# Performance work log

Measured on AMD Instinct MI355X. Metric: run time of the kernel, lower is better.

Reference implementation:

```python
import jax, jax.numpy as jnp
import numpy as np

D = 128        # hidden dim d
ED = 16        # edge_dim (Time2Vec width)
L = 2          # layers
N_BV, N_LT, N_CM, N_DN = 100000, 20000, 2000, 100000
E0, E1, E2, E3 = 600000, 200000, 500000, 200000
W_SCALE = 0.02


def setup_inputs() -> dict:
    key = jax.random.key(0)
    ks = jax.random.split(key, 24)
    rn = lambda i, s: jax.random.normal(ks[i], s, dtype=jnp.float32)
    ri = lambda i, e, hi: jax.random.randint(ks[i], (e,), 0, hi, dtype=jnp.int32)
    return {
        # node features per type
        "h_bv": rn(0, (N_BV, D)), "h_lt": rn(1, (N_LT, D)),
        "h_cm": rn(2, (N_CM, D)), "h_dn": rn(3, (N_DN, D)),
        # Time2Vec edge features per edge type
        "ft0": rn(4, (E0, ED)), "ft1": rn(5, (E1, ED)),
        "ft2": rn(6, (E2, ED)), "ft3": rn(7, (E3, ED)),
        # per-layer, per-edge-type conv Linear(2d, d)
        "conv_W": rn(8, (L, 4, 2 * D, D)) * W_SCALE,
        "conv_b": jnp.zeros((L, 4, D), jnp.float32),
        # per-edge-type edge MLP Linear(edge_dim, d)
        "emlp_W": rn(9, (4, ED, D)) * W_SCALE,
        "emlp_b": jnp.zeros((4, D), jnp.float32),
        # per-node-type LayerNorm params (order: bv, lt, cm, dn)
        "ln_g": jnp.ones((4, D), jnp.float32),
        "ln_b": jnp.zeros((4, D), jnp.float32),
        # edge indices (src -> dst): voted_on lt->bv, rev_read cm->bv,
        # donated_to dn->lt, read bv->cm
        "src0": ri(10, E0, N_LT), "dst0": ri(11, E0, N_BV),
        "src1": ri(12, E1, N_CM), "dst1": ri(13, E1, N_BV),
        "src2": ri(14, E2, N_DN), "dst2": ri(15, E2, N_LT),
        "src3": ri(16, E3, N_BV), "dst3": ri(17, E3, N_CM),
    }


def _seg_mean(x, idx, n):
    # scatter_mean: segment sum divided by counts (empty segments -> 0)
    s = jax.ops.segment_sum(x, idx, num_segments=n)
    c = jax.ops.segment_sum(jnp.ones((idx.shape[0],), x.dtype), idx, num_segments=n)
    return s / jnp.maximum(c, 1.0)[:, None]


def _layernorm(x, g, b, eps=1e-5):
    m = jnp.mean(x, -1, keepdims=True)
    v = jnp.var(x, -1, keepdims=True)
    return (x - m) * jax.lax.rsqrt(v + eps) * g + b


def reference(h_bv, h_lt, h_cm, h_dn, ft0, ft1, ft2, ft3,
              conv_W, conv_b, emlp_W, emlp_b, ln_g, ln_b,
              src0, dst0, src1, dst1, src2, dst2, src3, dst3):
    # node-type order: 0=bill_version, 1=legislator_term, 2=committee, 3=donor
    h = [h_bv, h_lt, h_cm, h_dn]
    # (et_idx, src_nt, dst_nt, src_idx, dst_idx, edge_time_feat)
    edges = [(0, 1, 0, src0, dst0, ft0),
             (1, 2, 0, src1, dst1, ft1),
             (2, 3, 1, src2, dst2, ft2),
             (3, 0, 2, src3, dst3, ft3)]
    n_layers = conv_W.shape[0]
    for l in range(n_layers):
        out = [jnp.zeros_like(x) for x in h]
        for (e, si, di, src, dst, ft) in edges:
            n_dst = h[di].shape[0]
            agg = _seg_mean(h[si][src], dst, n_dst)          # [N_dst, d]
            cat = jnp.concatenate([h[di], agg], axis=-1)     # [N_dst, 2d]
            y = cat @ conv_W[l, e] + conv_b[l, e]            # [N_dst, d]
            bias = ft @ emlp_W[e] + emlp_b[e]                # [E, d]
            y = y + _seg_mean(bias, dst, n_dst)
            out[di] = out[di] + y
        # drop=0.0 -> dropout is identity
        h = [_layernorm(out[i], ln_g[i], ln_b[i]) for i in range(4)]
    return tuple(h)
```

## Files before the change

### kernel.cpp

```cpp
#include <hip/hip_runtime.h>

typedef short v8s __attribute__((ext_vector_type(8)));
typedef float v4f __attribute__((ext_vector_type(4)));

#define S_I 100352

#define DEG_B   0ull
#define OFF_B   1605632ull
#define CUR_B   3211264ull
#define CSRS_B  4816896ull
#define FTS_B   16817152ull
#define BSUM_B  31025152ull
#define BPRE_B  31033344ull
#define WT_B    31041536ull
#define WEXT_B  31500288ull
#define VROW_B  31598592ull
#define AEXT_B  31599104ull
#define HA_B    47215104ull
#define ZA_B    104047104ull
#define HO_B    160879104ull
#define WS_NEEDED 192111104ull

__device__ __forceinline__ unsigned short f2bf(float f) {
    unsigned u = __float_as_uint(f);
    u += 0x7fffu + ((u >> 16) & 1u);
    return (unsigned short)(u >> 16);
}
__device__ __forceinline__ float bf2f(unsigned short h) {
    return __uint_as_float(((unsigned)h) << 16);
}

struct IPtr4 { const int* p[4]; };
struct IPtr8 { const int* s[4]; const int* d[4]; };
struct FPtr4 { const float* p[4]; };

__device__ __forceinline__ void edec(const IPtr8& sd, int i, int& li, int& eo,
                                     int& cb, int& d, int& s) {
    if (i < 600000)       { li = i;           eo = 0;       cb = 0;       d = sd.d[0][li]; s = sd.s[0][li]; }
    else if (i < 800000)  { li = i - 600000;  eo = 600000;  cb = S_I;     d = sd.d[1][li]; s = sd.s[1][li]; }
    else if (i < 1300000) { li = i - 800000;  eo = 800000;  cb = 2 * S_I; d = sd.d[2][li]; s = sd.s[2][li]; }
    else                  { li = i - 1300000; eo = 1300000; cb = 3 * S_I; d = sd.d[3][li]; s = sd.s[3][li]; }
}

__global__ void hist(IPtr4 dst, int* __restrict__ deg) {
    int base = blockIdx.x * 256 + threadIdx.x;
    if (base >= 375000) return;
    int d[4], cb[4];
#pragma unroll
    for (int k = 0; k < 4; k++) {
        int i = base + 375000 * k;
        if (i < 600000)       { cb[k] = 0;       d[k] = dst.p[0][i]; }
        else if (i < 800000)  { cb[k] = S_I;     d[k] = dst.p[1][i - 600000]; }
        else if (i < 1300000) { cb[k] = 2 * S_I; d[k] = dst.p[2][i - 800000]; }
        else                  { cb[k] = 3 * S_I; d[k] = dst.p[3][i - 1300000]; }
    }
#pragma unroll
    for (int k = 0; k < 4; k++) atomicAdd(&deg[cb[k] + d[k]], 1);
}

__device__ __forceinline__ void blk_decode(int b, int& e, int& lb, int& N) {
    if (b < 98)       { e = 0; lb = b;       N = 100000; }
    else if (b < 196) { e = 1; lb = b - 98;  N = 100000; }
    else if (b < 216) { e = 2; lb = b - 196; N = 20000;  }
    else              { e = 3; lb = b - 216; N = 2000;   }
}

__global__ void scan_p1(const int* __restrict__ deg, int* __restrict__ bsum) {
    int tid = threadIdx.x;
    int e, lb, N;
    blk_decode(blockIdx.x, e, lb, N);
    const int* dg = deg + e * S_I;
    int base = lb * 1024 + tid * 4;
    int s = 0;
#pragma unroll
    for (int j = 0; j < 4; j++) { int i = base + j; if (i < N) s += dg[i]; }
    for (int o = 32; o > 0; o >>= 1) s += __shfl_down(s, o);
    __shared__ int wsm[4];
    if ((tid & 63) == 0) wsm[tid >> 6] = s;
    __syncthreads();
    if (tid == 0) bsum[e * 512 + lb] = wsm[0] + wsm[1] + wsm[2] + wsm[3];
}

__global__ void scan_p2(const int* __restrict__ bsum, int* __restrict__ bpre, int* __restrict__ off) {
    __shared__ int sh[256];
    int tid = threadIdx.x;
    for (int e = 0; e < 4; e++) {
        int nb = (e < 2) ? 98 : (e == 2 ? 20 : 2);
        int N  = (e < 2) ? 100000 : (e == 2 ? 20000 : 2000);
        int v = (tid < nb) ? bsum[e * 512 + tid] : 0;
        sh[tid] = v;
        __syncthreads();
        for (int s = 1; s < 256; s <<= 1) {
            int t = (tid >= s) ? sh[tid - s] : 0;
            __syncthreads();
            sh[tid] += t;
            __syncthreads();
        }
        if (tid < nb) bpre[e * 512 + tid] = sh[tid] - v;
        if (tid == 0) off[e * S_I + N] = sh[255];
        __syncthreads();
    }
}

__global__ void scan_p3(const int* __restrict__ deg, const int* __restrict__ bpre,
                        int* __restrict__ off, int* __restrict__ cur) {
    int tid = threadIdx.x;
    int e, lb, N;
    blk_decode(blockIdx.x, e, lb, N);
    const int* dg = deg + e * S_I;
    int base = lb * 1024 + tid * 4;
    int v[4], s = 0;
#pragma unroll
    for (int j = 0; j < 4; j++) { int i = base + j; v[j] = (i < N) ? dg[i] : 0; s += v[j]; }
    int lane = tid & 63, w = tid >> 6;
    int sc = s;
    for (int d = 1; d < 64; d <<= 1) { int t = __shfl_up(sc, d); if (lane >= d) sc += t; }
    __shared__ int wsm[4];
    if (lane == 63) wsm[w] = sc;
    __syncthreads();
    int wpre = 0;
    for (int ww = 0; ww < 4; ww++) if (ww < w) wpre += wsm[ww];
    int run = bpre[e * 512 + lb] + wpre + (sc - s);
#pragma unroll
    for (int j = 0; j < 4; j++) {
        int i = base + j;
        if (i < N) { off[e * S_I + i] = run; cur[e * S_I + i] = run; }
        run += v[j];
    }
}

__global__ void fillcsr2(IPtr8 sd, int* __restrict__ cur, int2* __restrict__ csr2) {
    int base = blockIdx.x * 256 + threadIdx.x;
    if (base >= 375000) return;
    int li[4], eo[4], cb[4], d[4], s[4];
#pragma unroll
    for (int k = 0; k < 4; k++)
        edec(sd, base + 375000 * k, li[k], eo[k], cb[k], d[k], s[k]);
    int p[4];
#pragma unroll
    for (int k = 0; k < 4; k++)
        p[k] = atomicAdd(&cur[cb[k] + d[k]], 1);
#pragma unroll
    for (int k = 0; k < 4; k++)
        csr2[eo[k] + p[k]] = make_int2(s[k], li[k]);
}

__global__ __launch_bounds__(256) void ft_gather3(const int* __restrict__ off,
        const int2* __restrict__ csr2, FPtr4 ft, float* __restrict__ fts) {
    long long gid = (long long)blockIdx.x * 256 + threadIdx.x;
    int rid = (int)(gid >> 4), k = (int)(gid & 15);
    if (rid >= 222000) return;
    int e, n, eo;
    if (rid < 100000)      { e = 0; n = rid;          eo = 0; }
    else if (rid < 200000) { e = 1; n = rid - 100000; eo = 600000; }
    else if (rid < 220000) { e = 2; n = rid - 200000; eo = 800000; }
    else                   { e = 3; n = rid - 220000; eo = 1300000; }
    int s = off[e * S_I + n], en = off[e * S_I + n + 1];
    int dg = en - s;
    const int2* ep = csr2 + eo + s;
    const float* fp = ft.p[e];
    float a0 = 0.f, a1 = 0.f, a2 = 0.f, a3 = 0.f;
    int j = 0;
    for (; j + 4 <= dg; j += 4) {
        int e0 = ep[j].y, e1 = ep[j + 1].y, e2 = ep[j + 2].y, e3 = ep[j + 3].y;
        a0 += fp[(long long)e0 * 16 + k];
        a1 += fp[(long long)e1 * 16 + k];
        a2 += fp[(long long)e2 * 16 + k];
        a3 += fp[(long long)e3 * 16 + k];
    }
    if (j + 2 <= dg) {
        int e0 = ep[j].y, e1 = ep[j + 1].y;
        a0 += fp[(long long)e0 * 16 + k];
        a1 += fp[(long long)e1 * 16 + k];
        j += 2;
    }
    if (j < dg) a2 += fp[(long long)ep[j].y * 16 + k];
    fts[(long long)rid * 16 + k] = (a0 + a1) + (a2 + a3);
}

__global__ void const_build(const float* __restrict__ convW, const float* __restrict__ emlpW,
                            const float* __restrict__ emlpb, const float* __restrict__ convb,
                            const float* __restrict__ lnb, unsigned short* __restrict__ wt,
                            unsigned short* __restrict__ wext, float* __restrict__ vrow) {
    int gid = blockIdx.x * 256 + threadIdx.x;
    if (gid < 229376) {
        int i = gid;
        int l = i / 114688;
        int rem = i - l * 114688;
        int slot = rem >> 14;
        int idx = rem & 16383;
        int c = idx >> 7, k = idx & 127;
        float v;
        if (slot < 4)
            v = convW[((size_t)(l * 4 + slot) * 256 + 128 + k) * 128 + c];
        else if (slot == 4)
            v = convW[((size_t)(l * 4 + 0) * 256 + k) * 128 + c] +
                convW[((size_t)(l * 4 + 1) * 256 + k) * 128 + c];
        else
            v = convW[((size_t)(l * 4 + (slot - 3)) * 256 + k) * 128 + c];
        wt[i] = f2bf(v);
    } else if (gid < 229376 + 49152) {
        int g = gid - 229376;
        int slot = g >> 13;
        int rem = g & 8191;
        int c = rem >> 6, r = rem & 63;
        int l = slot / 3, t = slot - l * 3;
        int ef = (t == 0) ? 0 : (t == 1) ? 2 : 3;
        int rr = r & 31, half = r >> 5;
        int e = (t == 0) ? (half ? 1 : 0) : (half ? -1 : ef);
        float v = 0.f;
        if (e >= 0) {
            if (rr < 16)       v = emlpW[e * 2048 + rr * 128 + c];
            else if (rr == 16) v = emlpb[e * 128 + c];
        }
        if (r == 62) {
            v = convb[(l * 4 + ef) * 128 + c];
            if (t == 0) v += convb[(l * 4 + 1) * 128 + c];
        }
        wext[(long long)slot * 8192 + c * 64 + r] = f2bf(v);
    } else if (gid < 229376 + 49152 + 128) {
        int c = gid - 229376 - 49152;
        float s = 0.f;
        for (int k = 0; k < 128; k++)
            s += bf2f(f2bf(lnb[384 + k])) * bf2f(f2bf(convW[((size_t)(1 * 4 + 2) * 256 + 128 + k) * 128 + c]));
        vrow[c] = s;
    }
}

__global__ void aext_build(const int* __restrict__ off, const float* __restrict__ fts,
                           unsigned short* __restrict__ aext) {
    int gid = blockIdx.x * 256 + threadIdx.x;
    if (gid >= 7808000) return;
    int wid = gid >> 6, c = gid & 63;
    int t, n;
    if (wid < 100000)      { t = 0; n = wid; }
    else if (wid < 120000) { t = 1; n = wid - 100000; }
    else                   { t = 2; n = wid - 120000; }
    int cc = c & 31, half = c >> 5;
    int e = -1;
    if (t == 0) e = half ? 1 : 0;
    else if (half == 0) e = (t == 1) ? 2 : 3;
    float v = 0.f;
    if (e >= 0) {
        int s = off[e * S_I + n], en = off[e * S_I + n + 1];
        int dg = en - s;
        if (dg > 0) {
            int fb = (e == 0) ? 0 : (e == 1) ? 100000 : (e == 2) ? 200000 : 220000;
            if (cc < 16)       v = fts[(long long)(fb + n) * 16 + cc] / (float)dg;
            else if (cc == 16) v = 1.f;
        }
    }
    if (c == 62) v = 1.f;
    aext[(long long)wid * 64 + c] = f2bf(v);
}

__global__ void h0cvt(FPtr4 h, unsigned short* __restrict__ ha) {
    long long i4 = ((long long)blockIdx.x * 256 + threadIdx.x) * 4;
    if (i4 >= 28416000ll) return;
    long long r = i4 >> 7;
    int c = (int)(i4 & 127);
    int t; long long lr;
    if (r < 100000)      { t = 0; lr = r; }
    else if (r < 120000) { t = 1; lr = r - 100000; }
    else if (r < 122000) { t = 2; lr = r - 120000; }
    else                 { t = 3; lr = r - 122000; }
    const float4 v = *(const float4*)&h.p[t][lr * 128 + c];
    ushort4 o;
    o.x = f2bf(v.x); o.y = f2bf(v.y); o.z = f2bf(v.z); o.w = f2bf(v.w);
    *(ushort4*)&ha[i4] = o;
}

__device__ __forceinline__ void acc8(float* t, uint4 v) {
    t[0] += __uint_as_float(v.x << 16);
    t[1] += __uint_as_float(v.x & 0xffff0000u);
    t[2] += __uint_as_float(v.y << 16);
    t[3] += __uint_as_float(v.y & 0xffff0000u);
    t[4] += __uint_as_float(v.z << 16);
    t[5] += __uint_as_float(v.z & 0xffff0000u);
    t[6] += __uint_as_float(v.w << 16);
    t[7] += __uint_as_float(v.w & 0xffff0000u);
}

__global__ __launch_bounds__(256) void pull_all(int l, const int* __restrict__ off,
        const int2* __restrict__ csr2, const unsigned short* __restrict__ za,
        const float* __restrict__ vrow, unsigned short* __restrict__ hout) {
    long long gid = (long long)blockIdx.x * 256 + threadIdx.x;
    int wid = (int)(gid >> 6), lane = (int)(gid & 63);
    if (wid >= 122000) return;
    int t, n;
    if (wid < 100000)      { t = 0; n = wid; }
    else if (wid < 120000) { t = 1; n = wid - 100000; }
    else                   { t = 2; n = wid - 120000; }
    int sub = lane >> 4, k8 = (lane & 15) * 8;
    float a[8];
#pragma unroll
    for (int i = 0; i < 8; i++) a[i] = 0.f;
    int ef = (t == 0) ? 0 : (t == 1) ? 2 : 3;
    int ne = (t == 0) ? 2 : 1;
    for (int ii = 0; ii < ne; ii++) {
        int e = ef + ii;
        int s = off[e * S_I + n], en = off[e * S_I + n + 1];
        int cnt = en - s;
        if (cnt <= 0) continue;
        if (e == 2 && l == 1) {
            if (sub == 0) {
                float4 v0 = *(const float4*)&vrow[k8];
                float4 v1 = *(const float4*)&vrow[k8 + 4];
                a[0] += v0.x; a[1] += v0.y; a[2] += v0.z; a[3] += v0.w;
                a[4] += v1.x; a[5] += v1.y; a[6] += v1.z; a[7] += v1.w;
            }
            continue;
        }
        int eo   = (e == 0) ? 0 : (e == 1) ? 600000 : (e == 2) ? 800000 : 1300000;
        long long zo = (e == 0) ? 0 : (e == 1) ? 20000 : (e == 2) ? 22000 : 122000;
        const int2* cs = csr2 + eo + s;
        const unsigned short* zb = za + zo * 128;
        float t0[8], t1[8];
#pragma unroll
        for (int i = 0; i < 8; i++) { t0[i] = 0.f; t1[i] = 0.f; }
        int j = sub;
        for (; j + 4 < cnt; j += 8) {
            int i0 = cs[j].x, i1 = cs[j + 4].x;
            uint4 v0 = *(const uint4*)&zb[(long long)i0 * 128 + k8];
            uint4 v1 = *(const uint4*)&zb[(long long)i1 * 128 + k8];
            acc8(t0, v0);
            acc8(t1, v1);
        }
        if (j < cnt) {
            int i0 = cs[j].x;
            uint4 v0 = *(const uint4*)&zb[(long long)i0 * 128 + k8];
            acc8(t0, v0);
        }
        float inv = 1.f / (float)cnt;
#pragma unroll
        for (int i = 0; i < 8; i++) a[i] += (t0[i] + t1[i]) * inv;
    }
#pragma unroll
    for (int i = 0; i < 8; i++) {
        a[i] += __shfl_xor(a[i], 16);
        a[i] += __shfl_xor(a[i], 32);
    }
    if (sub == 0) {
        uint4 p;
        p.x = (unsigned)f2bf(a[0]) | ((unsigned)f2bf(a[1]) << 16);
        p.y = (unsigned)f2bf(a[2]) | ((unsigned)f2bf(a[3]) << 16);
        p.z = (unsigned)f2bf(a[4]) | ((unsigned)f2bf(a[5]) << 16);
        p.w = (unsigned)f2bf(a[6]) | ((unsigned)f2bf(a[7]) << 16);
        *(uint4*)&hout[(long long)wid * 128 + k8] = p;
    }
}

__global__ __launch_bounds__(256, 2) void zgemm(int l, const unsigned short* __restrict__ ha,
        const unsigned short* __restrict__ wt, unsigned short* __restrict__ za) {
    __shared__ unsigned short As[16384];
    __shared__ unsigned short Bs[16384];
    int b = blockIdx.x;
    int e, lb, M; long long aoff, zoff;
    if (l == 0) {
        if (b < 157)      { e = 0; lb = b;       M = 20000;  aoff = 100000; zoff = 0; }
        else if (b < 173) { e = 1; lb = b - 157; M = 2000;   aoff = 120000; zoff = 20000; }
        else if (b < 955) { e = 2; lb = b - 173; M = 100000; aoff = 122000; zoff = 22000; }
        else              { e = 3; lb = b - 955; M = 100000; aoff = 0;      zoff = 122000; }
    } else {
        if (b < 157)      { e = 0; lb = b;       M = 20000;  aoff = 100000; zoff = 0; }
        else if (b < 173) { e = 1; lb = b - 157; M = 2000;   aoff = 120000; zoff = 20000; }
        else              { e = 3; lb = b - 173; M = 100000; aoff = 0;      zoff = 122000; }
    }
    const unsigned short* A  = ha + aoff * 128;
    const unsigned short* Wt = wt + (size_t)(l * 7 + e) * 16384;
    unsigned short* outb = za + zoff * 128;
    int tid = threadIdx.x;
    long long row0 = (long long)lb * 128;
#pragma unroll
    for (int i = 0; i < 8; i++) {
        int idx = tid + i * 256;
        int m = idx >> 4, c = idx & 15;
        int sw = c ^ (m & 15);
        uint4 va = make_uint4(0u, 0u, 0u, 0u);
        long long gr = row0 + m;
        if (gr < M) va = *(const uint4*)&A[gr * 128 + c * 8];
        *(uint4*)&As[m * 128 + sw * 8] = va;
        uint4 wv = *(const uint4*)&Wt[m * 128 + c * 8];
        *(uint4*)&Bs[m * 128 + sw * 8] = wv;
    }
    __syncthreads();
    int lane = tid & 63, w = tid >> 6;
    int q = lane >> 4, ml = lane & 15;
    v4f acc[2][8];
#pragma unroll
    for (int i = 0; i < 2; i++)
#pragma unroll
        for (int j = 0; j < 8; j++) acc[i][j] = (v4f){0.f, 0.f, 0.f, 0.f};
#pragma unroll
    for (int kc = 0; kc < 4; kc++) {
        int ch = (4 * kc + q) ^ ml;
        v8s af[2], bf[8];
#pragma unroll
        for (int i = 0; i < 2; i++) af[i] = *(const v8s*)&As[(32 * w + 16 * i + ml) * 128 + ch * 8];
#pragma unroll
        for (int j = 0; j < 8; j++) bf[j] = *(const v8s*)&Bs[(16 * j + ml) * 128 + ch * 8];
#pragma unroll
        for (int i = 0; i < 2; i++)
#pragma unroll
            for (int j = 0; j < 8; j++)
                acc[i][j] = __builtin_amdgcn_mfma_f32_16x16x32_bf16(af[i], bf[j], acc[i][j], 0, 0, 0);
    }
#pragma unroll
    for (int i = 0; i < 2; i++)
#pragma unroll
        for (int r = 0; r < 4; r++) {
            long long row = row0 + 32 * w + 16 * i + q * 4 + r;
            if (row < M) {
#pragma unroll
                for (int j = 0; j < 8; j++)
                    outb[row * 128 + 16 * j + ml] = f2bf(acc[i][j][r]);
            }
        }
}

__global__ __launch_bounds__(256, 2) void selfgemm(int l, unsigned short* __restrict__ ha,
        const unsigned short* __restrict__ wt, const unsigned short* __restrict__ wext,
        const unsigned short* __restrict__ aext, const unsigned short* __restrict__ ho,
        float* __restrict__ outf, const float* __restrict__ lng, const float* __restrict__ lnb) {
    __shared__ unsigned short As[16384];
    __shared__ unsigned short Bs[16384];
    int b = blockIdx.x;
    int t, lb, M; long long hoff;
    if (b < 782)      { t = 0; lb = b;       M = 100000; hoff = 0; }
    else if (b < 939) { t = 1; lb = b - 782; M = 20000;  hoff = 100000; }
    else              { t = 2; lb = b - 939; M = 2000;   hoff = 120000; }
    const unsigned short* A    = ha + hoff * 128;
    const unsigned short* Ax   = aext + hoff * 64;
    const unsigned short* Wt_  = wt + (size_t)(l * 7 + 4 + t) * 16384;
    const unsigned short* Wx   = wext + (size_t)(l * 3 + t) * 8192;
    const unsigned short* Cadd = ho + hoff * 128;
    const float* g  = lng + t * 128;
    const float* bb = lnb + t * 128;
    int tid = threadIdx.x;
    long long row0 = (long long)lb * 128;
#pragma unroll
    for (int i = 0; i < 8; i++) {
        int idx = tid + i * 256;
        int m = idx >> 4, c = idx & 15;
        int sw = c ^ (m & 15);
        uint4 va = make_uint4(0u, 0u, 0u, 0u);
        long long gr = row0 + m;
        if (gr < M) va = *(const uint4*)&A[gr * 128 + c * 8];
        *(uint4*)&As[m * 128 + sw * 8] = va;
        uint4 wv = *(const uint4*)&Wt_[m * 128 + c * 8];
        *(uint4*)&Bs[m * 128 + sw * 8] = wv;
    }
    __syncthreads();
    int lane = tid & 63, w = tid >> 6;
    int q = lane >> 4, ml = lane & 15;
    v4f acc[2][8];
#pragma unroll
    for (int i = 0; i < 2; i++)
#pragma unroll
        for (int j = 0; j < 8; j++) acc[i][j] = (v4f){0.f, 0.f, 0.f, 0.f};
#pragma unroll
    for (int kc = 0; kc < 4; kc++) {
        int ch = (4 * kc + q) ^ ml;
        v8s af[2], bf[8];
#pragma unroll
        for (int i = 0; i < 2; i++) af[i] = *(const v8s*)&As[(32 * w + 16 * i + ml) * 128 + ch * 8];
#pragma unroll
        for (int j = 0; j < 8; j++) bf[j] = *(const v8s*)&Bs[(16 * j + ml) * 128 + ch * 8];
#pragma unroll
        for (int i = 0; i < 2; i++)
#pragma unroll
            for (int j = 0; j < 8; j++)
                acc[i][j] = __builtin_amdgcn_mfma_f32_16x16x32_bf16(af[i], bf[j], acc[i][j], 0, 0, 0);
    }
    __syncthreads();
#pragma unroll
    for (int i = 0; i < 4; i++) {
        int idx = tid + i * 256;
        int m = idx >> 3, c = idx & 7;
        int sw = c ^ (m & 7);
        uint4 va = make_uint4(0u, 0u, 0u, 0u);
        long long gr = row0 + m;
        if (gr < M) va = *(const uint4*)&Ax[gr * 64 + c * 8];
        *(uint4*)&As[m * 64 + sw * 8] = va;
        uint4 wv = *(const uint4*)&Wx[m * 64 + c * 8];
        *(uint4*)&Bs[m * 64 + sw * 8] = wv;
    }
    __syncthreads();
#pragma unroll
    for (int kc = 0; kc < 2; kc++) {
        int ch = (4 * kc + q) ^ (ml & 7);
        v8s af[2], bf[8];
#pragma unroll
        for (int i = 0; i < 2; i++) af[i] = *(const v8s*)&As[(32 * w + 16 * i + ml) * 64 + ch * 8];
#pragma unroll
        for (int j = 0; j < 8; j++) bf[j] = *(const v8s*)&Bs[(16 * j + ml) * 64 + ch * 8];
#pragma unroll
        for (int i = 0; i < 2; i++)
#pragma unroll
            for (int j = 0; j < 8; j++)
                acc[i][j] = __builtin_amdgcn_mfma_f32_16x16x32_bf16(af[i], bf[j], acc[i][j], 0, 0, 0);
    }
    float gv[8], bv[8];
#pragma unroll
    for (int j = 0; j < 8; j++) { gv[j] = g[16 * j + ml]; bv[j] = bb[16 * j + ml]; }
    unsigned short* outb = ha + hoff * 128;
    float* outF = outf + hoff * 128;
#pragma unroll
    for (int i = 0; i < 2; i++) {
#pragma unroll
        for (int r = 0; r < 4; r++) {
            long long row = row0 + 32 * w + 16 * i + q * 4 + r;
            bool valid = row < M;
            float s = 0.f, s2 = 0.f;
#pragma unroll
            for (int j = 0; j < 8; j++) {
                float v = acc[i][j][r];
                if (valid) v += bf2f(Cadd[row * 128 + 16 * j + ml]);
                acc[i][j][r] = v;
                s += v; s2 += v * v;
            }
#pragma unroll
            for (int msk = 1; msk < 16; msk <<= 1) {
                s  += __shfl_xor(s,  msk);
                s2 += __shfl_xor(s2, msk);
            }
            float mean = s * 0.0078125f;
            float var  = s2 * 0.0078125f - mean * mean;
            float rs = rsqrtf(var + 1e-5f);
            if (valid) {
#pragma unroll
                for (int j = 0; j < 8; j++) {
                    float v = (acc[i][j][r] - mean) * rs * gv[j] + bv[j];
                    if (l == 0) outb[row * 128 + 16 * j + ml] = f2bf(v);
                    else        outF[row * 128 + 16 * j + ml] = v;
                }
            }
        }
    }
}

__global__ void fill_dn(float* __restrict__ of, const float* __restrict__ lnb3) {
    long long i4 = ((long long)blockIdx.x * 256 + threadIdx.x) * 4;
    if (i4 >= 12800000ll) return;
    int c = (int)(i4 & 127);
    *(float4*)&of[i4] = make_float4(lnb3[c], lnb3[c + 1], lnb3[c + 2], lnb3[c + 3]);
}

extern "C" void kernel_launch(void* const* d_in, const int* in_sizes, int n_in,
                              void* d_out, int out_size, void* d_ws, size_t ws_size,
                              hipStream_t stream) {
    if (ws_size < WS_NEEDED) return;

    const float* h0[4] = {(const float*)d_in[0], (const float*)d_in[1],
                          (const float*)d_in[2], (const float*)d_in[3]};
    const float* ftp[4] = {(const float*)d_in[4], (const float*)d_in[5],
                           (const float*)d_in[6], (const float*)d_in[7]};
    const float* convW = (const float*)d_in[8];
    const float* convb = (const float*)d_in[9];
    const float* emlpW = (const float*)d_in[10];
    const float* emlpb = (const float*)d_in[11];
    const float* lng   = (const float*)d_in[12];
    const float* lnb   = (const float*)d_in[13];
    const int* srcp[4] = {(const int*)d_in[14], (const int*)d_in[16],
                          (const int*)d_in[18], (const int*)d_in[20]};
    const int* dstp[4] = {(const int*)d_in[15], (const int*)d_in[17],
                          (const int*)d_in[19], (const int*)d_in[21]};
    char* ws = (char*)d_ws;
    float* out = (float*)d_out;

    int* deg = (int*)(ws + DEG_B);
    int* off = (int*)(ws + OFF_B);
    int* cur = (int*)(ws + CUR_B);
    int2* csr2 = (int2*)(ws + CSRS_B);
    float* fts = (float*)(ws + FTS_B);
    int* bsum = (int*)(ws + BSUM_B);
    int* bpre = (int*)(ws + BPRE_B);
    unsigned short* wt   = (unsigned short*)(ws + WT_B);
    unsigned short* wext = (unsigned short*)(ws + WEXT_B);
    float* vrow = (float*)(ws + VROW_B);
    unsigned short* aext = (unsigned short*)(ws + AEXT_B);
    unsigned short* ha = (unsigned short*)(ws + HA_B);
    unsigned short* za = (unsigned short*)(ws + ZA_B);
    unsigned short* ho = (unsigned short*)(ws + HO_B);

    hipMemsetAsync(deg, 0, 4 * S_I * sizeof(int), stream);

    IPtr4 dsts; for (int e = 0; e < 4; e++) dsts.p[e] = dstp[e];
    hist<<<1465, 256, 0, stream>>>(dsts, deg);

    scan_p1<<<218, 256, 0, stream>>>(deg, bsum);
    scan_p2<<<1, 256, 0, stream>>>(bsum, bpre, off);
    scan_p3<<<218, 256, 0, stream>>>(deg, bpre, off, cur);
    IPtr8 sd;
    for (int e = 0; e < 4; e++) { sd.s[e] = srcp[e]; sd.d[e] = dstp[e]; }
    fillcsr2<<<1465, 256, 0, stream>>>(sd, cur, csr2);

    FPtr4 ftq;  for (int e = 0; e < 4; e++) ftq.p[e] = ftp[e];
    ft_gather3<<<13875, 256, 0, stream>>>(off, csr2, ftq, fts);

    const_build<<<1089, 256, 0, stream>>>(convW, emlpW, emlpb, convb, lnb, wt, wext, vrow);
    FPtr4 hq; for (int t = 0; t < 4; t++) hq.p[t] = h0[t];
    h0cvt<<<27750, 256, 0, stream>>>(hq, ha);
    aext_build<<<30500, 256, 0, stream>>>(off, fts, aext);

    for (int l = 0; l < 2; l++) {
        zgemm<<<(l == 0) ? 1737 : 955, 256, 0, stream>>>(l, ha, wt, za);
        pull_all<<<30500, 256, 0, stream>>>(l, off, csr2, za, vrow, ho);
        selfgemm<<<955, 256, 0, stream>>>(l, ha, wt, wext, aext, ho, out, lng, lnb);
    }
    fill_dn<<<12500, 256, 0, stream>>>(out + 122000ll * 128, lnb + 384);
}
```

Baseline: 887.2 us.

## Merge independent stages into combined kernels to cut launches and overlap work

```diff
diff --git a/kernel.cpp b/kernel.cpp
--- a/kernel.cpp
+++ b/kernel.cpp
@@ -34,14 +34,6 @@
 struct IPtr8 { const int* s[4]; const int* d[4]; };
 struct FPtr4 { const float* p[4]; };
 
-__device__ __forceinline__ void edec(const IPtr8& sd, int i, int& li, int& eo,
-                                     int& cb, int& d, int& s) {
-    if (i < 600000)       { li = i;           eo = 0;       cb = 0;       d = sd.d[0][li]; s = sd.s[0][li]; }
-    else if (i < 800000)  { li = i - 600000;  eo = 600000;  cb = S_I;     d = sd.d[1][li]; s = sd.s[1][li]; }
-    else if (i < 1300000) { li = i - 800000;  eo = 800000;  cb = 2 * S_I; d = sd.d[2][li]; s = sd.s[2][li]; }
-    else                  { li = i - 1300000; eo = 1300000; cb = 3 * S_I; d = sd.d[3][li]; s = sd.s[3][li]; }
-}
-
 __global__ void hist(IPtr4 dst, int* __restrict__ deg) {
     int base = blockIdx.x * 256 + threadIdx.x;
     if (base >= 375000) return;
@@ -129,107 +121,280 @@
     }
 }
 
-__global__ void fillcsr2(IPtr8 sd, int* __restrict__ cur, int2* __restrict__ csr2) {
-    int base = blockIdx.x * 256 + threadIdx.x;
-    if (base >= 375000) return;
-    int li[4], eo[4], cb[4], d[4], s[4];
-#pragma unroll
-    for (int k = 0; k < 4; k++)
-        edec(sd, base + 375000 * k, li[k], eo[k], cb[k], d[k], s[k]);
-    int p[4];
-#pragma unroll
-    for (int k = 0; k < 4; k++)
-        p[k] = atomicAdd(&cur[cb[k] + d[k]], 1);
-#pragma unroll
-    for (int k = 0; k < 4; k++)
-        csr2[eo[k] + p[k]] = make_int2(s[k], li[k]);
-}
-
-__global__ __launch_bounds__(256) void ft_gather3(const int* __restrict__ off,
-        const int2* __restrict__ csr2, FPtr4 ft, float* __restrict__ fts) {
-    long long gid = (long long)blockIdx.x * 256 + threadIdx.x;
-    int rid = (int)(gid >> 4), k = (int)(gid & 15);
-    if (rid >= 222000) return;
-    int e, n, eo;
-    if (rid < 100000)      { e = 0; n = rid;          eo = 0; }
-    else if (rid < 200000) { e = 1; n = rid - 100000; eo = 600000; }
-    else if (rid < 220000) { e = 2; n = rid - 200000; eo = 800000; }
-    else                   { e = 3; n = rid - 220000; eo = 1300000; }
-    int s = off[e * S_I + n], en = off[e * S_I + n + 1];
-    int dg = en - s;
-    const int2* ep = csr2 + eo + s;
-    const float* fp = ft.p[e];
-    float a0 = 0.f, a1 = 0.f, a2 = 0.f, a3 = 0.f;
-    int j = 0;
-    for (; j + 4 <= dg; j += 4) {
-        int e0 = ep[j].y, e1 = ep[j + 1].y, e2 = ep[j + 2].y, e3 = ep[j + 3].y;
-        a0 += fp[(long long)e0 * 16 + k];
-        a1 += fp[(long long)e1 * 16 + k];
-        a2 += fp[(long long)e2 * 16 + k];
-        a3 += fp[(long long)e3 * 16 + k];
-    }
-    if (j + 2 <= dg) {
-        int e0 = ep[j].y, e1 = ep[j + 1].y;
-        a0 += fp[(long long)e0 * 16 + k];
-        a1 += fp[(long long)e1 * 16 + k];
-        j += 2;
-    }
-    if (j < dg) a2 += fp[(long long)ep[j].y * 16 + k];
-    fts[(long long)rid * 16 + k] = (a0 + a1) + (a2 + a3);
-}
-
-__global__ void const_build(const float* __restrict__ convW, const float* __restrict__ emlpW,
-                            const float* __restrict__ emlpb, const float* __restrict__ convb,
-                            const float* __restrict__ lnb, unsigned short* __restrict__ wt,
-                            unsigned short* __restrict__ wext, float* __restrict__ vrow) {
-    int gid = blockIdx.x * 256 + threadIdx.x;
-    if (gid < 229376) {
-        int i = gid;
-        int l = i / 114688;
-        int rem = i - l * 114688;
-        int slot = rem >> 14;
-        int idx = rem & 16383;
-        int c = idx >> 7, k = idx & 127;
-        float v;
-        if (slot < 4)
-            v = convW[((size_t)(l * 4 + slot) * 256 + 128 + k) * 128 + c];
-        else if (slot == 4)
-            v = convW[((size_t)(l * 4 + 0) * 256 + k) * 128 + c] +
-                convW[((size_t)(l * 4 + 1) * 256 + k) * 128 + c];
-        else
-            v = convW[((size_t)(l * 4 + (slot - 3)) * 256 + k) * 128 + c];
-        wt[i] = f2bf(v);
-    } else if (gid < 229376 + 49152) {
-        int g = gid - 229376;
-        int slot = g >> 13;
-        int rem = g & 8191;
-        int c = rem >> 6, r = rem & 63;
-        int l = slot / 3, t = slot - l * 3;
-        int ef = (t == 0) ? 0 : (t == 1) ? 2 : 3;
-        int rr = r & 31, half = r >> 5;
-        int e = (t == 0) ? (half ? 1 : 0) : (half ? -1 : ef);
-        float v = 0.f;
-        if (e >= 0) {
-            if (rr < 16)       v = emlpW[e * 2048 + rr * 128 + c];
-            else if (rr == 16) v = emlpb[e * 128 + c];
-        }
-        if (r == 62) {
-            v = convb[(l * 4 + ef) * 128 + c];
-            if (t == 0) v += convb[(l * 4 + 1) * 128 + c];
-        }
-        wext[(long long)slot * 8192 + c * 64 + r] = f2bf(v);
-    } else if (gid < 229376 + 49152 + 128) {
-        int c = gid - 229376 - 49152;
-        float s = 0.f;
-        for (int k = 0; k < 128; k++)
-            s += bf2f(f2bf(lnb[384 + k])) * bf2f(f2bf(convW[((size_t)(1 * 4 + 2) * 256 + 128 + k) * 128 + c]));
-        vrow[c] = s;
-    }
-}
-
-__global__ void aext_build(const int* __restrict__ off, const float* __restrict__ fts,
-                           unsigned short* __restrict__ aext) {
-    int gid = blockIdx.x * 256 + threadIdx.x;
+__global__ void mega1(IPtr8 sd, int* __restrict__ cur, int2* __restrict__ csr2,
+                      FPtr4 h, unsigned short* __restrict__ ha,
+                      const float* __restrict__ convW, const float* __restrict__ emlpW,
+                      const float* __restrict__ emlpb, const float* __restrict__ convb,
+                      const float* __restrict__ lnb, unsigned short* __restrict__ wt,
+                      unsigned short* __restrict__ wext, float* __restrict__ vrow) {
+    int b = blockIdx.x;
+    int tid = threadIdx.x;
+    if (b < 1465) {
+        int base = b * 256 + tid;
+        if (base >= 375000) return;
+        int li[4], eo[4], cb[4], d[4], s[4];
+#pragma unroll
+        for (int k = 0; k < 4; k++) {
+            int i = base + 375000 * k;
+            if (i < 600000)       { li[k] = i;           eo[k] = 0;       cb[k] = 0;       d[k] = sd.d[0][li[k]]; s[k] = sd.s[0][li[k]]; }
+            else if (i < 800000)  { li[k] = i - 600000;  eo[k] = 600000;  cb[k] = S_I;     d[k] = sd.d[1][li[k]]; s[k] = sd.s[1][li[k]]; }
+            else if (i < 1300000) { li[k] = i - 800000;  eo[k] = 800000;  cb[k] = 2 * S_I; d[k] = sd.d[2][li[k]]; s[k] = sd.s[2][li[k]]; }
+            else                  { li[k] = i - 1300000; eo[k] = 1300000; cb[k] = 3 * S_I; d[k] = sd.d[3][li[k]]; s[k] = sd.s[3][li[k]]; }
+        }
+        int p[4];
+#pragma unroll
+        for (int k = 0; k < 4; k++)
+            p[k] = atomicAdd(&cur[cb[k] + d[k]], 1);
+#pragma unroll
+        for (int k = 0; k < 4; k++)
+            csr2[eo[k] + p[k]] = make_int2(s[k], li[k]);
+    } else if (b < 29215) {
+        long long i4 = ((long long)(b - 1465) * 256 + tid) * 4;
+        if (i4 >= 28416000ll) return;
+        long long r = i4 >> 7;
+        int c = (int)(i4 & 127);
+        int t; long long lr;
+        if (r < 100000)      { t = 0; lr = r; }
+        else if (r < 120000) { t = 1; lr = r - 100000; }
+        else if (r < 122000) { t = 2; lr = r - 120000; }
+        else                 { t = 3; lr = r - 122000; }
+        const float4 v = *(const float4*)&h.p[t][lr * 128 + c];
+        ushort4 o;
+        o.x = f2bf(v.x); o.y = f2bf(v.y); o.z = f2bf(v.z); o.w = f2bf(v.w);
+        *(ushort4*)&ha[i4] = o;
+    } else {
+        int gid = (b - 29215) * 256 + tid;
+        if (gid < 229376) {
+            int i = gid;
+            int l = i / 114688;
+            int rem = i - l * 114688;
+            int slot = rem >> 14;
+            int idx = rem & 16383;
+            int c = idx >> 7, k = idx & 127;
+            float v;
+            if (slot < 4)
+                v = convW[((size_t)(l * 4 + slot) * 256 + 128 + k) * 128 + c];
+            else if (slot == 4)
+                v = convW[((size_t)(l * 4 + 0) * 256 + k) * 128 + c] +
+                    convW[((size_t)(l * 4 + 1) * 256 + k) * 128 + c];
+            else
+                v = convW[((size_t)(l * 4 + (slot - 3)) * 256 + k) * 128 + c];
+            wt[i] = f2bf(v);
+        } else if (gid < 229376 + 49152) {
+            int g = gid - 229376;
+            int slot = g >> 13;
+            int rem = g & 8191;
+            int c = rem >> 6, r = rem & 63;
+            int l = slot / 3, t = slot - l * 3;
+            int ef = (t == 0) ? 0 : (t == 1) ? 2 : 3;
+            int rr = r & 31, half = r >> 5;
+            int e = (t == 0) ? (half ? 1 : 0) : (half ? -1 : ef);
+            float v = 0.f;
+            if (e >= 0) {
+                if (rr < 16)       v = emlpW[e * 2048 + rr * 128 + c];
+                else if (rr == 16) v = emlpb[e * 128 + c];
+            }
+            if (r == 62) {
+                v = convb[(l * 4 + ef) * 128 + c];
+                if (t == 0) v += convb[(l * 4 + 1) * 128 + c];
+            }
+            wext[(long long)slot * 8192 + c * 64 + r] = f2bf(v);
+        } else if (gid < 229376 + 49152 + 128) {
+            int c = gid - 229376 - 49152;
+            float s = 0.f;
+            for (int k = 0; k < 128; k++)
+                s += bf2f(f2bf(lnb[384 + k])) * bf2f(f2bf(convW[((size_t)(1 * 4 + 2) * 256 + 128 + k) * 128 + c]));
+            vrow[c] = s;
+        }
+    }
+}
+
+__global__ __launch_bounds__(256, 2) void mega2(const unsigned short* __restrict__ ha,
+        const unsigned short* __restrict__ wt, unsigned short* __restrict__ za,
+        const int* __restrict__ off, const int2* __restrict__ csr2,
+        FPtr4 ft, float* __restrict__ fts) {
+    __shared__ unsigned short As[16384];
+    __shared__ unsigned short Bs[16384];
+    int tid = threadIdx.x;
+    if (blockIdx.x >= 1737) {
+        long long gid = (long long)(blockIdx.x - 1737) * 256 + tid;
+        int rid = (int)(gid >> 4), k = (int)(gid & 15);
+        if (rid >= 222000) return;
+        int e, n, eo;
+        if (rid < 100000)      { e = 0; n = rid;          eo = 0; }
+        else if (rid < 200000) { e = 1; n = rid - 100000; eo = 600000; }
+        else if (rid < 220000) { e = 2; n = rid - 200000; eo = 800000; }
+        else                   { e = 3; n = rid - 220000; eo = 1300000; }
+        int s = off[e * S_I + n], en = off[e * S_I + n + 1];
+        int dg = en - s;
+        const int2* ep = csr2 + eo + s;
+        const float* fp = ft.p[e];
+        float a0 = 0.f, a1 = 0.f, a2 = 0.f, a3 = 0.f;
+        int j = 0;
+        for (; j + 4 <= dg; j += 4) {
+            int e0 = ep[j].y, e1 = ep[j + 1].y, e2 = ep[j + 2].y, e3 = ep[j + 3].y;
+            a0 += fp[(long long)e0 * 16 + k];
+            a1 += fp[(long long)e1 * 16 + k];
+            a2 += fp[(long long)e2 * 16 + k];
+            a3 += fp[(long long)e3 * 16 + k];
+        }
+        if (j + 2 <= dg) {
+            int e0 = ep[j].y, e1 = ep[j + 1].y;
+            a0 += fp[(long long)e0 * 16 + k];
+            a1 += fp[(long long)e1 * 16 + k];
+            j += 2;
+        }
+        if (j < dg) a2 += fp[(long long)ep[j].y * 16 + k];
+        fts[(long long)rid * 16 + k] = (a0 + a1) + (a2 + a3);
+        return;
+    }
+    int b = blockIdx.x;
+    int e, lb, M; long long aoff, zoff;
+    if (b < 157)      { e = 0; lb = b;       M = 20000;  aoff = 100000; zoff = 0; }
+    else if (b < 173) { e = 1; lb = b - 157; M = 2000;   aoff = 120000; zoff = 20000; }
+    else if (b < 955) { e = 2; lb = b - 173; M = 100000; aoff = 122000; zoff = 22000; }
+    else              { e = 3; lb = b - 955; M = 100000; aoff = 0;      zoff = 122000; }
+    const unsigned short* A  = ha + aoff * 128;
+    const unsigned short* Wt = wt + (size_t)e * 16384;
+    unsigned short* outb = za + zoff * 128;
+    long long row0 = (long long)lb * 128;
+#pragma unroll
+    for (int i = 0; i < 8; i++) {
+        int idx = tid + i * 256;
+        int m = idx >> 4, c = idx & 15;
+        int sw = c ^ (m & 15);
+        uint4 va = make_uint4(0u, 0u, 0u, 0u);
+        long long gr = row0 + m;
+        if (gr < M) va = *(const uint4*)&A[gr * 128 + c * 8];
+        *(uint4*)&As[m * 128 + sw * 8] = va;
+        uint4 wv = *(const uint4*)&Wt[m * 128 + c * 8];
+        *(uint4*)&Bs[m * 128 + sw * 8] = wv;
+    }
+    __syncthreads();
+    int lane = tid & 63, w = tid >> 6;
+    int q = lane >> 4, ml = lane & 15;
+    v4f acc[2][8];
+#pragma unroll
+    for (int i = 0; i < 2; i++)
+#pragma unroll
+        for (int j = 0; j < 8; j++) acc[i][j] = (v4f){0.f, 0.f, 0.f, 0.f};
+#pragma unroll
+    for (int kc = 0; kc < 4; kc++) {
+        int ch = (4 * kc + q) ^ ml;
+        v8s af[2], bf[8];
+#pragma unroll
+        for (int i = 0; i < 2; i++) af[i] = *(const v8s*)&As[(32 * w + 16 * i + ml) * 128 + ch * 8];
+#pragma unroll
+        for (int j = 0; j < 8; j++) bf[j] = *(const v8s*)&Bs[(16 * j + ml) * 128 + ch * 8];
+#pragma unroll
+        for (int i = 0; i < 2; i++)
+#pragma unroll
+            for (int j = 0; j < 8; j++)
+                acc[i][j] = __builtin_amdgcn_mfma_f32_16x16x32_bf16(af[i], bf[j], acc[i][j], 0, 0, 0);
+    }
+#pragma unroll
+    for (int i = 0; i < 2; i++)
+#pragma unroll
+        for (int r = 0; r < 4; r++) {
+            long long row = row0 + 32 * w + 16 * i + q * 4 + r;
+            if (row < M) {
+#pragma unroll
+                for (int j = 0; j < 8; j++)
+                    outb[row * 128 + 16 * j + ml] = f2bf(acc[i][j][r]);
+            }
+        }
+}
+
+__device__ __forceinline__ void acc8(float* t, uint4 v) {
+    t[0] += __uint_as_float(v.x << 16);
+    t[1] += __uint_as_float(v.x & 0xffff0000u);
+    t[2] += __uint_as_float(v.y << 16);
+    t[3] += __uint_as_float(v.y & 0xffff0000u);
+    t[4] += __uint_as_float(v.z << 16);
+    t[5] += __uint_as_float(v.z & 0xffff0000u);
+    t[6] += __uint_as_float(v.w << 16);
+    t[7] += __uint_as_float(v.w & 0xffff0000u);
+}
+
+__device__ __forceinline__ void pull_body(int l, int vb, int tid, const int* __restrict__ off,
+        const int2* __restrict__ csr2, const unsigned short* __restrict__ za,
+        const float* __restrict__ vrow, unsigned short* __restrict__ hout) {
+    long long gid = (long long)vb * 256 + tid;
+    int wid = (int)(gid >> 6), lane = (int)(gid & 63);
+    if (wid >= 122000) return;
+    int t, n;
+    if (wid < 100000)      { t = 0; n = wid; }
+    else if (wid < 120000) { t = 1; n = wid - 100000; }
+    else                   { t = 2; n = wid - 120000; }
+    int sub = lane >> 4, k8 = (lane & 15) * 8;
+    float a[8];
+#pragma unroll
+    for (int i = 0; i < 8; i++) a[i] = 0.f;
+    int ef = (t == 0) ? 0 : (t == 1) ? 2 : 3;
+    int ne = (t == 0) ? 2 : 1;
+    for (int ii = 0; ii < ne; ii++) {
+        int e = ef + ii;
+        int s = off[e * S_I + n], en = off[e * S_I + n + 1];
+        int cnt = en - s;
+        if (cnt <= 0) continue;
+        if (e == 2 && l == 1) {
+            if (sub == 0) {
+                float4 v0 = *(const float4*)&vrow[k8];
+                float4 v1 = *(const float4*)&vrow[k8 + 4];
+                a[0] += v0.x; a[1] += v0.y; a[2] += v0.z; a[3] += v0.w;
+                a[4] += v1.x; a[5] += v1.y; a[6] += v1.z; a[7] += v1.w;
+            }
+            continue;
+        }
+        int eo   = (e == 0) ? 0 : (e == 1) ? 600000 : (e == 2) ? 800000 : 1300000;
+        long long zo = (e == 0) ? 0 : (e == 1) ? 20000 : (e == 2) ? 22000 : 122000;
+        const int2* cs = csr2 + eo + s;
+        const unsigned short* zb = za + zo * 128;
+        float t0[8], t1[8];
+#pragma unroll
+        for (int i = 0; i < 8; i++) { t0[i] = 0.f; t1[i] = 0.f; }
+        int j = sub;
+        for (; j + 4 < cnt; j += 8) {
+            int i0 = cs[j].x, i1 = cs[j + 4].x;
+            uint4 v0 = *(const uint4*)&zb[(long long)i0 * 128 + k8];
+            uint4 v1 = *(const uint4*)&zb[(long long)i1 * 128 + k8];
+            acc8(t0, v0);
+            acc8(t1, v1);
+        }
+        if (j < cnt) {
+            int i0 = cs[j].x;
+            uint4 v0 = *(const uint4*)&zb[(long long)i0 * 128 + k8];
+            acc8(t0, v0);
+        }
+        float inv = 1.f / (float)cnt;
+#pragma unroll
+        for (int i = 0; i < 8; i++) a[i] += (t0[i] + t1[i]) * inv;
+    }
+#pragma unroll
+    for (int i = 0; i < 8; i++) {
+        a[i] += __shfl_xor(a[i], 16);
+        a[i] += __shfl_xor(a[i], 32);
+    }
+    if (sub == 0) {
+        uint4 p;
+        p.x = (unsigned)f2bf(a[0]) | ((unsigned)f2bf(a[1]) << 16);
+        p.y = (unsigned)f2bf(a[2]) | ((unsigned)f2bf(a[3]) << 16);
+        p.z = (unsigned)f2bf(a[4]) | ((unsigned)f2bf(a[5]) << 16);
+        p.w = (unsigned)f2bf(a[6]) | ((unsigned)f2bf(a[7]) << 16);
+        *(uint4*)&hout[(long long)wid * 128 + k8] = p;
+    }
+}
+
+__global__ __launch_bounds__(256) void mega3(const int* __restrict__ off,
+        const int2* __restrict__ csr2, const unsigned short* __restrict__ za,
+        const float* __restrict__ vrow, unsigned short* __restrict__ ho,
+        const float* __restrict__ fts, unsigned short* __restrict__ aext) {
+    int tid = threadIdx.x;
+    if (blockIdx.x < 30500) {
+        pull_body(0, blockIdx.x, tid, off, csr2, za, vrow, ho);
+        return;
+    }
+    int gid = (blockIdx.x - 30500) * 256 + tid;
     if (gid >= 7808000) return;
     int wid = gid >> 6, c = gid & 63;
     int t, n;
@@ -254,100 +419,19 @@
     aext[(long long)wid * 64 + c] = f2bf(v);
 }
 
-__global__ void h0cvt(FPtr4 h, unsigned short* __restrict__ ha) {
-    long long i4 = ((long long)blockIdx.x * 256 + threadIdx.x) * 4;
-    if (i4 >= 28416000ll) return;
-    long long r = i4 >> 7;
+__global__ __launch_bounds__(256) void mega4(const int* __restrict__ off,
+        const int2* __restrict__ csr2, const unsigned short* __restrict__ za,
+        const float* __restrict__ vrow, unsigned short* __restrict__ ho,
+        float* __restrict__ of_dn, const float* __restrict__ lnb3) {
+    int tid = threadIdx.x;
+    if (blockIdx.x < 30500) {
+        pull_body(1, blockIdx.x, tid, off, csr2, za, vrow, ho);
+        return;
+    }
+    long long i4 = ((long long)(blockIdx.x - 30500) * 256 + tid) * 4;
+    if (i4 >= 12800000ll) return;
     int c = (int)(i4 & 127);
-    int t; long long lr;
-    if (r < 100000)      { t = 0; lr = r; }
-    else if (r < 120000) { t = 1; lr = r - 100000; }
-    else if (r < 122000) { t = 2; lr = r - 120000; }
-    else                 { t = 3; lr = r - 122000; }
-    const float4 v = *(const float4*)&h.p[t][lr * 128 + c];
-    ushort4 o;
-    o.x = f2bf(v.x); o.y = f2bf(v.y); o.z = f2bf(v.z); o.w = f2bf(v.w);
-    *(ushort4*)&ha[i4] = o;
-}
-
-__device__ __forceinline__ void acc8(float* t, uint4 v) {
-    t[0] += __uint_as_float(v.x << 16);
-    t[1] += __uint_as_float(v.x & 0xffff0000u);
-    t[2] += __uint_as_float(v.y << 16);
-    t[3] += __uint_as_float(v.y & 0xffff0000u);
-    t[4] += __uint_as_float(v.z << 16);
-    t[5] += __uint_as_float(v.z & 0xffff0000u);
-    t[6] += __uint_as_float(v.w << 16);
-    t[7] += __uint_as_float(v.w & 0xffff0000u);
-}
-
-__global__ __launch_bounds__(256) void pull_all(int l, const int* __restrict__ off,
-        const int2* __restrict__ csr2, const unsigned short* __restrict__ za,
-        const float* __restrict__ vrow, unsigned short* __restrict__ hout) {
-    long long gid = (long long)blockIdx.x * 256 + threadIdx.x;
-    int wid = (int)(gid >> 6), lane = (int)(gid & 63);
-    if (wid >= 122000) return;
-    int t, n;
-    if (wid < 100000)      { t = 0; n = wid; }
-    else if (wid < 120000) { t = 1; n = wid - 100000; }
-    else                   { t = 2; n = wid - 120000; }
-    int sub = lane >> 4, k8 = (lane & 15) * 8;
-    float a[8];
-#pragma unroll
-    for (int i = 0; i < 8; i++) a[i] = 0.f;
-    int ef = (t == 0) ? 0 : (t == 1) ? 2 : 3;
-    int ne = (t == 0) ? 2 : 1;
-    for (int ii = 0; ii < ne; ii++) {
-        int e = ef + ii;
-        int s = off[e * S_I + n], en = off[e * S_I + n + 1];
-        int cnt = en - s;
-        if (cnt <= 0) continue;
-        if (e == 2 && l == 1) {
-            if (sub == 0) {
-                float4 v0 = *(const float4*)&vrow[k8];
-                float4 v1 = *(const float4*)&vrow[k8 + 4];
-                a[0] += v0.x; a[1] += v0.y; a[2] += v0.z; a[3] += v0.w;
-                a[4] += v1.x; a[5] += v1.y; a[6] += v1.z; a[7] += v1.w;
-            }
-            continue;
-        }
-        int eo   = (e == 0) ? 0 : (e == 1) ? 600000 : (e == 2) ? 800000 : 1300000;
-        long long zo = (e == 0) ? 0 : (e == 1) ? 20000 : (e == 2) ? 22000 : 122000;
-        const int2* cs = csr2 + eo + s;
-        const unsigned short* zb = za + zo * 128;
-        float t0[8], t1[8];
-#pragma unroll
-        for (int i = 0; i < 8; i++) { t0[i] = 0.f; t1[i] = 0.f; }
-        int j = sub;
-        for (; j + 4 < cnt; j += 8) {
-            int i0 = cs[j].x, i1 = cs[j + 4].x;
-            uint4 v0 = *(const uint4*)&zb[(long long)i0 * 128 + k8];
-            uint4 v1 = *(const uint4*)&zb[(long long)i1 * 128 + k8];
-            acc8(t0, v0);
-            acc8(t1, v1);
-        }
-        if (j < cnt) {
-            int i0 = cs[j].x;
-            uint4 v0 = *(const uint4*)&zb[(long long)i0 * 128 + k8];
-            acc8(t0, v0);
-        }
-        float inv = 1.f / (float)cnt;
-#pragma unroll
-        for (int i = 0; i < 8; i++) a[i] += (t0[i] + t1[i]) * inv;
-    }
-#pragma unroll
-    for (int i = 0; i < 8; i++) {
-        a[i] += __shfl_xor(a[i], 16);
-        a[i] += __shfl_xor(a[i], 32);
-    }
-    if (sub == 0) {
-        uint4 p;
-        p.x = (unsigned)f2bf(a[0]) | ((unsigned)f2bf(a[1]) << 16);
-        p.y = (unsigned)f2bf(a[2]) | ((unsigned)f2bf(a[3]) << 16);
-        p.z = (unsigned)f2bf(a[4]) | ((unsigned)f2bf(a[5]) << 16);
-        p.w = (unsigned)f2bf(a[6]) | ((unsigned)f2bf(a[7]) << 16);
-        *(uint4*)&hout[(long long)wid * 128 + k8] = p;
-    }
+    *(float4*)&of_dn[i4] = make_float4(lnb3[c], lnb3[c + 1], lnb3[c + 2], lnb3[c + 3]);
 }
 
 __global__ __launch_bounds__(256, 2) void zgemm(int l, const unsigned short* __restrict__ ha,
@@ -356,16 +440,9 @@
     __shared__ unsigned short Bs[16384];
     int b = blockIdx.x;
     int e, lb, M; long long aoff, zoff;
-    if (l == 0) {
-        if (b < 157)      { e = 0; lb = b;       M = 20000;  aoff = 100000; zoff = 0; }
-        else if (b < 173) { e = 1; lb = b - 157; M = 2000;   aoff = 120000; zoff = 20000; }
-        else if (b < 955) { e = 2; lb = b - 173; M = 100000; aoff = 122000; zoff = 22000; }
-        else              { e = 3; lb = b - 955; M = 100000; aoff = 0;      zoff = 122000; }
-    } else {
-        if (b < 157)      { e = 0; lb = b;       M = 20000;  aoff = 100000; zoff = 0; }
-        else if (b < 173) { e = 1; lb = b - 157; M = 2000;   aoff = 120000; zoff = 20000; }
-        else              { e = 3; lb = b - 173; M = 100000; aoff = 0;      zoff = 122000; }
-    }
+    if (b < 157)      { e = 0; lb = b;       M = 20000;  aoff = 100000; zoff = 0; }
+    else if (b < 173) { e = 1; lb = b - 157; M = 2000;   aoff = 120000; zoff = 20000; }
+    else              { e = 3; lb = b - 173; M = 100000; aoff = 0;      zoff = 122000; }
     const unsigned short* A  = ha + aoff * 128;
     const unsigned short* Wt = wt + (size_t)(l * 7 + e) * 16384;
     unsigned short* outb = za + zoff * 128;
@@ -539,13 +616,6 @@
     }
 }
 
-__global__ void fill_dn(float* __restrict__ of, const float* __restrict__ lnb3) {
-    long long i4 = ((long long)blockIdx.x * 256 + threadIdx.x) * 4;
-    if (i4 >= 12800000ll) return;
-    int c = (int)(i4 & 127);
-    *(float4*)&of[i4] = make_float4(lnb3[c], lnb3[c + 1], lnb3[c + 2], lnb3[c + 3]);
-}
-
 extern "C" void kernel_launch(void* const* d_in, const int* in_sizes, int n_in,
                               void* d_out, int out_size, void* d_ws, size_t ws_size,
                               hipStream_t stream) {
@@ -591,22 +661,24 @@
     scan_p1<<<218, 256, 0, stream>>>(deg, bsum);
     scan_p2<<<1, 256, 0, stream>>>(bsum, bpre, off);
     scan_p3<<<218, 256, 0, stream>>>(deg, bpre, off, cur);
+
     IPtr8 sd;
     for (int e = 0; e < 4; e++) { sd.s[e] = srcp[e]; sd.d[e] = dstp[e]; }
-    fillcsr2<<<1465, 256, 0, stream>>>(sd, cur, csr2);
+    FPtr4 hq; for (int t = 0; t < 4; t++) hq.p[t] = h0[t];
+    mega1<<<30304, 256, 0, stream>>>(sd, cur, csr2, hq, ha,
+                                     convW, emlpW, emlpb, convb, lnb, wt, wext, vrow);
 
     FPtr4 ftq;  for (int e = 0; e < 4; e++) ftq.p[e] = ftp[e];
-    ft_gather3<<<13875, 256, 0, stream>>>(off, csr2, ftq, fts);
-
-    const_build<<<1089, 256, 0, stream>>>(convW, emlpW, emlpb, convb, lnb, wt, wext, vrow);
-    FPtr4 hq; for (int t = 0; t < 4; t++) hq.p[t] = h0[t];
-    h0cvt<<<27750, 256, 0, stream>>>(hq, ha);
-    aext_build<<<30500, 256, 0, stream>>>(off, fts, aext);
-
-    for (int l = 0; l < 2; l++) {
-        zgemm<<<(l == 0) ? 1737 : 955, 256, 0, stream>>>(l, ha, wt, za);
-        pull_all<<<30500, 256, 0, stream>>>(l, off, csr2, za, vrow, ho);
-        selfgemm<<<955, 256, 0, stream>>>(l, ha, wt, wext, aext, ho, out, lng, lnb);
-    }
-    fill_dn<<<12500, 256, 0, stream>>>(out + 122000ll * 128, lnb + 384);
-}
+    mega2<<<15612, 256, 0, stream>>>(ha, wt, za, off, csr2, ftq, fts);
+
+    mega3<<<61000, 256, 0, stream>>>(off, csr2, za, vrow, ho, fts, aext);
+
+    selfgemm<<<955, 256, 0, stream>>>(0, ha, wt, wext, aext, ho, out, lng, lnb);
+
+    zgemm<<<955, 256, 0, stream>>>(1, ha, wt, za);
+
+    mega4<<<43000, 256, 0, stream>>>(off, csr2, za, vrow, ho,
+                                     out + 122000ll * 128, lnb + 384);
+
+    selfgemm<<<955, 256, 0, stream>>>(1, ha, wt, wext, aext, ho, out, lng, lnb);
+}
```

After: 931.3 us. 1.05x slower.
